# Optimization experiments

Measured on AMD Instinct MI355X. Metric: run time of the kernel, lower is better.

Reference implementation:

```python
import jax, jax.numpy as jnp
import numpy as np

MAX_SP = 180.0
MAX_TP = 365.0
NUM_HEADS = 4
HEAD_SIZE = 32
ALL_HEAD = NUM_HEADS * HEAD_SIZE  # 128
HIDDEN = 256
FIRE_H = 32


def _fire(dist, c, w1, w2, max_dist):
    # dist: (B,N); w1: (FIRE_H,1); w2: (1,FIRE_H)
    d = dist[..., None].astype(jnp.float32)
    c = jnp.maximum(c, 0.0)
    d = jnp.log(c * d + 1.0) / jnp.log(c * max_dist + 1.0)
    h = jax.nn.silu(d @ w1.T)          # (B,N,FIRE_H)
    return (h @ w2.T)[..., 0]          # (B,N)


def setup_inputs() -> dict:
    key = jax.random.key(0)
    ks = jax.random.split(key, 20)
    B, S, N, C = 8, 256, 128, 64
    inp = {
        "source_ids": jax.random.randint(ks[0], (B, S, N), 0, 2),
        "source_cluster_labels": jax.random.randint(ks[1], (B, N), 0, C),
        "in_cluster_spatial_dist": jax.random.uniform(ks[2], (B, N), dtype=jnp.float32),
        "in_cluster_temporal_dist": jax.random.uniform(ks[3], (B, N), dtype=jnp.float32),
        "num_clusters": C,
        # FIRE spatial params
        "c_sp": jnp.asarray(100.0, jnp.float32),
        "sp_w1": 0.1 * jax.random.normal(ks[4], (FIRE_H, 1), jnp.float32),
        "sp_w2": 0.1 * jax.random.normal(ks[5], (1, FIRE_H), jnp.float32),
        # FIRE temporal params
        "c_tp": jnp.asarray(100.0, jnp.float32),
        "tp_w1": 0.1 * jax.random.normal(ks[6], (FIRE_H, 1), jnp.float32),
        "tp_w2": 0.1 * jax.random.normal(ks[7], (1, FIRE_H), jnp.float32),
        # attention_weights: Linear(1, num_heads)
        "attn_w": 0.1 * jax.random.normal(ks[8], (NUM_HEADS,), jnp.float32),
        "attn_b": 0.1 * jax.random.normal(ks[9], (NUM_HEADS,), jnp.float32),
        # value: Linear(1, all_head_size)
        "val_w": 0.1 * jax.random.normal(ks[10], (ALL_HEAD,), jnp.float32),
        "val_b": 0.1 * jax.random.normal(ks[11], (ALL_HEAD,), jnp.float32),
        # ffn: Linear(all_head_size, hidden)
        "ffn_w": 0.05 * jax.random.normal(ks[12], (HIDDEN, ALL_HEAD), jnp.float32),
        "ffn_b": 0.05 * jax.random.normal(ks[13], (HIDDEN,), jnp.float32),
    }
    return inp


def reference(source_ids, source_cluster_labels, in_cluster_spatial_dist,
              in_cluster_temporal_dist, num_clusters,
              c_sp, sp_w1, sp_w2, c_tp, tp_w1, tp_w2,
              attn_w, attn_b, val_w, val_b, ffn_w, ffn_b):
    B, S, N = source_ids.shape
    C = num_clusters
    # FIRE distance biases over source sites: (B,N)
    bias = (_fire(in_cluster_spatial_dist, c_sp, sp_w1, sp_w2, MAX_SP)
            + _fire(in_cluster_temporal_dist, c_tp, tp_w1, tp_w2, MAX_TP))
    x = source_ids.astype(jnp.float32)                 # (B,S,N)
    attn_logits = x[..., None] * attn_w + attn_b       # (B,S,N,H)
    v = (x[..., None] * val_w + val_b).reshape(B, S, N, NUM_HEADS, HEAD_SIZE)
    attn_logits = attn_logits + bias[:, None, :, None]
    member = jax.nn.one_hot(source_cluster_labels, C, dtype=jnp.float32)  # (B,N,C)
    non_member = (1.0 - member)[:, None, :, None, :] * -1e9               # (B,1,N,1,C)
    masked = attn_logits[..., None] + non_member       # (B,S,N,H,C)
    probs = jnp.nan_to_num(jax.nn.softmax(masked, axis=2))
    # pool members per cluster: (B,S,C,H,head_size)
    pooled = jnp.einsum('bsnhc,bsnhd->bschd', probs, v).reshape(B, S, C, ALL_HEAD)
    out = pooled @ ffn_w.T + ffn_b                     # (B,S,C,HIDDEN)
    has_member = jnp.any(member > 0, axis=1)           # (B,C)
    return out * has_member[:, None, :, None].astype(out.dtype)
```

## Files before the change

kernel.cpp:

```cpp
#include <hip/hip_runtime.h>
#include <hip/hip_bf16.h>

#define NB 8
#define NS 256
#define NN 128
#define NC 64
#define NH 4
#define AH 128
#define HID 256
#define FH 32

typedef float f32x4 __attribute__((ext_vector_type(4)));


__global__ __launch_bounds__(256) void fold_kernel(
    const float* __restrict__ val_w, const float* __restrict__ val_b,
    const float* __restrict__ ffn_w, const float* __restrict__ ffn_b,
    float* __restrict__ ws)
{
    __shared__ float sVw[AH], sVb[AH];
    const int t = threadIdx.x;
    if (t < AH) { sVw[t] = val_w[t]; sVb[t] = val_b[t]; }
    __syncthreads();

    const int o = t;
    const float4* fr = reinterpret_cast<const float4*>(ffn_w + o * AH);
    float c0 = ffn_b[o];
    float w[NH] = {0.f, 0.f, 0.f, 0.f};
    #pragma unroll
    for (int k4 = 0; k4 < AH / 4; ++k4) {
        const float4 f = fr[k4];
        const int k = k4 * 4;
        const int h = k >> 5;
        c0  = fmaf(f.x, sVb[k], fmaf(f.y, sVb[k+1], fmaf(f.z, sVb[k+2], fmaf(f.w, sVb[k+3], c0))));
        w[h] = fmaf(f.x, sVw[k], fmaf(f.y, sVw[k+1], fmaf(f.z, sVw[k+2], fmaf(f.w, sVw[k+3], w[h]))));
    }
    ws[1536 + o] = c0;
    *reinterpret_cast<float4*>(ws + 1792 + o * NH) = make_float4(w[0], w[1], w[2], w[3]);
}

__global__ __launch_bounds__(256) void out_kernel(
    const int* __restrict__ src,
    const int* __restrict__ labels,
    const float* __restrict__ sp_d, const float* __restrict__ tp_d,
    const float* __restrict__ c_sp_p, const float* __restrict__ sp_w1, const float* __restrict__ sp_w2,
    const float* __restrict__ c_tp_p, const float* __restrict__ tp_w1, const float* __restrict__ tp_w2,
    const float* __restrict__ attn_w,
    const float* __restrict__ ws,
    float* __restrict__ out)
{
    __shared__ float sE[NN], sEx0[NN], sEx1[NN];
    __shared__ int   sLab[NN];
    __shared__ float sPa[NC][NH], sPb[NC][NH];
    __shared__ float sHm[NC];

    const int blk = blockIdx.x;
    const int b  = blk >> 7;
    const int s0 = (blk & 127) * 2;
    const int t  = threadIdx.x;

    const int o0 = (t & 63) * 4;
    const int crow = t >> 6;
    const f32x4 c0v = *reinterpret_cast<const f32x4*>(ws + 1536 + o0);
    f32x4 wrow[4];
    #pragma unroll
    for (int i = 0; i < 4; ++i)
        wrow[i] = *reinterpret_cast<const f32x4*>(ws + 1792 + (size_t)(o0 + i) * NH);

    if (t < NN) {
        const float csp = fmaxf(c_sp_p[0], 0.0f);
        const float ctp = fmaxf(c_tp_p[0], 0.0f);
        const float dsp = sp_d[b * NN + t];
        const float dtp = tp_d[b * NN + t];
        const int   lab = labels[b * NN + t];
        const int   x0  = src[((size_t)(b * NS + s0))     * NN + t];
        const int   x1  = src[((size_t)(b * NS + s0 + 1)) * NN + t];
        const float dns = __logf(fmaf(csp, dsp, 1.0f)) / __logf(fmaf(csp, 180.0f, 1.0f));
        const float dnt = __logf(fmaf(ctp, dtp, 1.0f)) / __logf(fmaf(ctp, 365.0f, 1.0f));
        float bias_sp = 0.f, bias_tp = 0.f;
        #pragma unroll
        for (int j = 0; j < FH; ++j) {
            const float zs = dns * sp_w1[j];
            bias_sp += (zs / (1.0f + __expf(-zs))) * sp_w2[j];
            const float zt = dnt * tp_w1[j];
            bias_tp += (zt / (1.0f + __expf(-zt))) * tp_w2[j];
        }
        const float e = __expf(bias_sp + bias_tp);
        sE[t]   = e;
        sLab[t] = lab;
        sEx0[t] = x0 ? e : 0.f;
        sEx1[t] = x1 ? e : 0.f;
    }
    __syncthreads();

    {
        const int c = t >> 2, q = t & 3;
        float tS = 0.f, b0 = 0.f, b1 = 0.f;
        #pragma unroll
        for (int i = 0; i < 32; ++i) {
            const int n = (i << 2) | q;
            const bool m = (sLab[n] == c);
            tS += m ? sE[n]   : 0.f;
            b0 += m ? sEx0[n] : 0.f;
            b1 += m ? sEx1[n] : 0.f;
        }
        tS += __shfl_xor(tS, 1); tS += __shfl_xor(tS, 2);
        b0 += __shfl_xor(b0, 1); b0 += __shfl_xor(b0, 2);
        b1 += __shfl_xor(b1, 1); b1 += __shfl_xor(b1, 2);
        float p0 = 0.f, p1 = 0.f, hm = 0.f;
        if (tS > 0.f) {
            hm = 1.f;
            const float ew = __expf(attn_w[q]);
            p0 = (b0 * ew) / ((tS - b0) + b0 * ew);
            p1 = (b1 * ew) / ((tS - b1) + b1 * ew);
        }
        sPa[c][q] = p0;
        sPb[c][q] = p1;
        if (q == 0) sHm[c] = hm;
    }
    __syncthreads();

    float* orow0 = out + ((size_t)(b * NS + s0)) * (NC * HID);
    #pragma unroll
    for (int ss = 0; ss < 2; ++ss) {
        float* orow = orow0 + (size_t)ss * (NC * HID);
        #pragma unroll
        for (int ci = 0; ci < 16; ++ci) {
            const int c = ci * 4 + crow;
            const float* P = ss ? sPb[c] : sPa[c];
            const float p0 = P[0], p1 = P[1], p2 = P[2], p3 = P[3];
            const float hm = sHm[c];
            f32x4 val;
            #pragma unroll
            for (int i = 0; i < 4; ++i) {
                float v = c0v[i];
                v = fmaf(p0, wrow[i][0], v);
                v = fmaf(p1, wrow[i][1], v);
                v = fmaf(p2, wrow[i][2], v);
                val[i] = fmaf(p3, wrow[i][3], v) * hm;
            }
            __builtin_nontemporal_store(val, reinterpret_cast<f32x4*>(orow + (size_t)c * HID + o0));
        }
    }
}

extern "C" void kernel_launch(void* const* d_in, const int* in_sizes, int n_in,
                              void* d_out, int out_size, void* d_ws, size_t ws_size,
                              hipStream_t stream) {
    const int*   src    = (const int*)d_in[0];
    const int*   labels = (const int*)d_in[1];
    const float* sp_d   = (const float*)d_in[2];
    const float* tp_d   = (const float*)d_in[3];
    const float* c_sp   = (const float*)d_in[5];
    const float* sp_w1  = (const float*)d_in[6];
    const float* sp_w2  = (const float*)d_in[7];
    const float* c_tp   = (const float*)d_in[8];
    const float* tp_w1  = (const float*)d_in[9];
    const float* tp_w2  = (const float*)d_in[10];
    const float* attn_w = (const float*)d_in[11];
    const float* val_w  = (const float*)d_in[13];
    const float* val_b  = (const float*)d_in[14];
    const float* ffn_w  = (const float*)d_in[15];
    const float* ffn_b  = (const float*)d_in[16];
    float* ws = (float*)d_ws;
    float* out = (float*)d_out;

    fold_kernel<<<1, 256, 0, stream>>>(val_w, val_b, ffn_w, ffn_b, ws);
    out_kernel<<<NB * NS / 2, 256, 0, stream>>>(src, labels, sp_d, tp_d,
                                                c_sp, sp_w1, sp_w2,
                                                c_tp, tp_w1, tp_w2,
                                                attn_w, ws, out);
}
```

Baseline: 39.88 us.

## Fuse weight-fold into output kernel and process four sequence rows per block

Removes the separate single-block fold kernel launch and instead has every block recompute the folded FFN constants (ffn_w·val_b and per-head ffn_w·val_w sums) into shared memory. Each block now handles four sequence positions instead of two, halving the grid and amortizing the FIRE bias and cluster reductions over more rows. The output store switches from nontemporal to a regular store and the cluster-to-thread mapping changes. The trade-off is redundant reading of the 128 KB ffn_w matrix by all 512 blocks, which adds L2 traffic and per-block latency before any output is written.

```diff
diff --git a/kernel.cpp b/kernel.cpp
--- a/kernel.cpp
+++ b/kernel.cpp
@@ -9,63 +9,51 @@
 #define AH 128
 #define HID 256
 #define FH 32
+#define SPB 4
 
 typedef float f32x4 __attribute__((ext_vector_type(4)));
 
-
-__global__ __launch_bounds__(256) void fold_kernel(
-    const float* __restrict__ val_w, const float* __restrict__ val_b,
-    const float* __restrict__ ffn_w, const float* __restrict__ ffn_b,
-    float* __restrict__ ws)
-{
-    __shared__ float sVw[AH], sVb[AH];
-    const int t = threadIdx.x;
-    if (t < AH) { sVw[t] = val_w[t]; sVb[t] = val_b[t]; }
-    __syncthreads();
-
-    const int o = t;
-    const float4* fr = reinterpret_cast<const float4*>(ffn_w + o * AH);
-    float c0 = ffn_b[o];
-    float w[NH] = {0.f, 0.f, 0.f, 0.f};
-    #pragma unroll
-    for (int k4 = 0; k4 < AH / 4; ++k4) {
-        const float4 f = fr[k4];
-        const int k = k4 * 4;
-        const int h = k >> 5;
-        c0  = fmaf(f.x, sVb[k], fmaf(f.y, sVb[k+1], fmaf(f.z, sVb[k+2], fmaf(f.w, sVb[k+3], c0))));
-        w[h] = fmaf(f.x, sVw[k], fmaf(f.y, sVw[k+1], fmaf(f.z, sVw[k+2], fmaf(f.w, sVw[k+3], w[h]))));
-    }
-    ws[1536 + o] = c0;
-    *reinterpret_cast<float4*>(ws + 1792 + o * NH) = make_float4(w[0], w[1], w[2], w[3]);
-}
-
-__global__ __launch_bounds__(256) void out_kernel(
+__global__ __launch_bounds__(256) void fused_kernel(
     const int* __restrict__ src,
     const int* __restrict__ labels,
     const float* __restrict__ sp_d, const float* __restrict__ tp_d,
     const float* __restrict__ c_sp_p, const float* __restrict__ sp_w1, const float* __restrict__ sp_w2,
     const float* __restrict__ c_tp_p, const float* __restrict__ tp_w1, const float* __restrict__ tp_w2,
     const float* __restrict__ attn_w,
-    const float* __restrict__ ws,
+    const float* __restrict__ val_w, const float* __restrict__ val_b,
+    const float* __restrict__ ffn_w, const float* __restrict__ ffn_b,
     float* __restrict__ out)
 {
-    __shared__ float sE[NN], sEx0[NN], sEx1[NN];
+    __shared__ float sC0[HID];
+    __shared__ float sW[HID][NH];
+    __shared__ float sE[NN];
+    __shared__ float sEx[SPB][NN];
     __shared__ int   sLab[NN];
-    __shared__ float sPa[NC][NH], sPb[NC][NH];
+    __shared__ float sP[SPB][NC][NH];
     __shared__ float sHm[NC];
 
     const int blk = blockIdx.x;
-    const int b  = blk >> 7;
-    const int s0 = (blk & 127) * 2;
+    const int b  = blk >> 6;
+    const int s0 = (blk & 63) * SPB;
     const int t  = threadIdx.x;
 
-    const int o0 = (t & 63) * 4;
-    const int crow = t >> 6;
-    const f32x4 c0v = *reinterpret_cast<const f32x4*>(ws + 1536 + o0);
-    f32x4 wrow[4];
-    #pragma unroll
-    for (int i = 0; i < 4; ++i)
-        wrow[i] = *reinterpret_cast<const f32x4*>(ws + 1792 + (size_t)(o0 + i) * NH);
+    {
+        const int o = t;
+        const float4* fr = reinterpret_cast<const float4*>(ffn_w + (size_t)o * AH);
+        float c0 = ffn_b[o];
+        float w[NH] = {0.f, 0.f, 0.f, 0.f};
+        #pragma unroll 8
+        for (int k4 = 0; k4 < AH / 4; ++k4) {
+            const float4 f = fr[k4];
+            const int k = k4 * 4;
+            const int h = k >> 5;
+            c0  = fmaf(f.x, val_b[k], fmaf(f.y, val_b[k+1], fmaf(f.z, val_b[k+2], fmaf(f.w, val_b[k+3], c0))));
+            w[h] = fmaf(f.x, val_w[k], fmaf(f.y, val_w[k+1], fmaf(f.z, val_w[k+2], fmaf(f.w, val_w[k+3], w[h]))));
+        }
+        sC0[o] = c0;
+        #pragma unroll
+        for (int h = 0; h < NH; ++h) sW[o][h] = w[h];
+    }
 
     if (t < NN) {
         const float csp = fmaxf(c_sp_p[0], 0.0f);
@@ -73,8 +61,10 @@
         const float dsp = sp_d[b * NN + t];
         const float dtp = tp_d[b * NN + t];
         const int   lab = labels[b * NN + t];
-        const int   x0  = src[((size_t)(b * NS + s0))     * NN + t];
-        const int   x1  = src[((size_t)(b * NS + s0 + 1)) * NN + t];
+        int x[SPB];
+        #pragma unroll
+        for (int ss = 0; ss < SPB; ++ss)
+            x[ss] = src[((size_t)(b * NS + s0 + ss)) * NN + t];
         const float dns = __logf(fmaf(csp, dsp, 1.0f)) / __logf(fmaf(csp, 180.0f, 1.0f));
         const float dnt = __logf(fmaf(ctp, dtp, 1.0f)) / __logf(fmaf(ctp, 365.0f, 1.0f));
         float bias_sp = 0.f, bias_tp = 0.f;
@@ -88,47 +78,60 @@
         const float e = __expf(bias_sp + bias_tp);
         sE[t]   = e;
         sLab[t] = lab;
-        sEx0[t] = x0 ? e : 0.f;
-        sEx1[t] = x1 ? e : 0.f;
+        #pragma unroll
+        for (int ss = 0; ss < SPB; ++ss)
+            sEx[ss][t] = x[ss] ? e : 0.f;
     }
     __syncthreads();
 
     {
         const int c = t >> 2, q = t & 3;
-        float tS = 0.f, b0 = 0.f, b1 = 0.f;
+        float tS = 0.f, bs[SPB] = {0.f, 0.f, 0.f, 0.f};
         #pragma unroll
         for (int i = 0; i < 32; ++i) {
             const int n = (i << 2) | q;
             const bool m = (sLab[n] == c);
-            tS += m ? sE[n]   : 0.f;
-            b0 += m ? sEx0[n] : 0.f;
-            b1 += m ? sEx1[n] : 0.f;
+            tS += m ? sE[n] : 0.f;
+            #pragma unroll
+            for (int ss = 0; ss < SPB; ++ss)
+                bs[ss] += m ? sEx[ss][n] : 0.f;
         }
         tS += __shfl_xor(tS, 1); tS += __shfl_xor(tS, 2);
-        b0 += __shfl_xor(b0, 1); b0 += __shfl_xor(b0, 2);
-        b1 += __shfl_xor(b1, 1); b1 += __shfl_xor(b1, 2);
-        float p0 = 0.f, p1 = 0.f, hm = 0.f;
-        if (tS > 0.f) {
-            hm = 1.f;
-            const float ew = __expf(attn_w[q]);
-            p0 = (b0 * ew) / ((tS - b0) + b0 * ew);
-            p1 = (b1 * ew) / ((tS - b1) + b1 * ew);
+        #pragma unroll
+        for (int ss = 0; ss < SPB; ++ss) {
+            bs[ss] += __shfl_xor(bs[ss], 1);
+            bs[ss] += __shfl_xor(bs[ss], 2);
         }
-        sPa[c][q] = p0;
-        sPb[c][q] = p1;
-        if (q == 0) sHm[c] = hm;
+        const bool nz = (tS > 0.f);
+        const float ew = __expf(attn_w[q]);
+        #pragma unroll
+        for (int ss = 0; ss < SPB; ++ss) {
+            float p = 0.f;
+            if (nz) p = (bs[ss] * ew) / ((tS - bs[ss]) + bs[ss] * ew);
+            sP[ss][c][q] = p;
+        }
+        if (q == 0) sHm[c] = nz ? 1.f : 0.f;
     }
     __syncthreads();
 
+    const int o0 = (t & 63) * 4;
+    const int crow = t >> 6;
+    f32x4 c0v, wrow[4];
+    #pragma unroll
+    for (int i = 0; i < 4; ++i) {
+        c0v[i] = sC0[o0 + i];
+        wrow[i][0] = sW[o0 + i][0]; wrow[i][1] = sW[o0 + i][1];
+        wrow[i][2] = sW[o0 + i][2]; wrow[i][3] = sW[o0 + i][3];
+    }
     float* orow0 = out + ((size_t)(b * NS + s0)) * (NC * HID);
     #pragma unroll
-    for (int ss = 0; ss < 2; ++ss) {
+    for (int ss = 0; ss < SPB; ++ss) {
         float* orow = orow0 + (size_t)ss * (NC * HID);
         #pragma unroll
         for (int ci = 0; ci < 16; ++ci) {
-            const int c = ci * 4 + crow;
-            const float* P = ss ? sPb[c] : sPa[c];
-            const float p0 = P[0], p1 = P[1], p2 = P[2], p3 = P[3];
+            const int c = crow * 16 + ci;
+            const float p0 = sP[ss][c][0], p1 = sP[ss][c][1];
+            const float p2 = sP[ss][c][2], p3 = sP[ss][c][3];
             const float hm = sHm[c];
             f32x4 val;
             #pragma unroll
@@ -139,7 +142,7 @@
                 v = fmaf(p2, wrow[i][2], v);
                 val[i] = fmaf(p3, wrow[i][3], v) * hm;
             }
-            __builtin_nontemporal_store(val, reinterpret_cast<f32x4*>(orow + (size_t)c * HID + o0));
+            *reinterpret_cast<f32x4*>(orow + (size_t)c * HID + o0) = val;
         }
     }
 }
@@ -162,12 +165,11 @@
     const float* val_b  = (const float*)d_in[14];
     const float* ffn_w  = (const float*)d_in[15];
     const float* ffn_b  = (const float*)d_in[16];
-    float* ws = (float*)d_ws;
     float* out = (float*)d_out;
 
-    fold_kernel<<<1, 256, 0, stream>>>(val_w, val_b, ffn_w, ffn_b, ws);
-    out_kernel<<<NB * NS / 2, 256, 0, stream>>>(src, labels, sp_d, tp_d,
-                                                c_sp, sp_w1, sp_w2,
-                                                c_tp, tp_w1, tp_w2,
-                                                attn_w, ws, out);
+    fused_kernel<<<NB * NS / SPB, 256, 0, stream>>>(src, labels, sp_d, tp_d,
+                                                    c_sp, sp_w1, sp_w2,
+                                                    c_tp, tp_w1, tp_w2,
+                                                    attn_w, val_w, val_b,
+                                                    ffn_w, ffn_b, out);
 }
```

Result: no change. 39.24 us (-1.6%).
